# Kernel tuning notes

Hardware: AMD Instinct MI355X
Metric: run time of the kernel (lower is better)

## Reference

```python
import jax, jax.numpy as jnp
import numpy as np

N_NODES = 50000
N_EDGES = 1600000
NEG_SLOPE = 0.2


def setup_inputs() -> dict:
    key = jax.random.key(0)
    ks = jax.random.split(key, 11)
    s = 0.1  # small init scale
    return {
        "x": jax.random.normal(ks[0], (N_NODES, 128), dtype=jnp.float32),
        "edge_index": jax.random.randint(ks[1], (2, N_EDGES), 0, N_NODES, dtype=jnp.int64),
        "W1": jax.random.normal(ks[2], (128, 128), dtype=jnp.float32) * s,
        "att_src1": jax.random.normal(ks[3], (2, 64), dtype=jnp.float32) * s,
        "att_dst1": jax.random.normal(ks[4], (2, 64), dtype=jnp.float32) * s,
        "b1": jax.random.normal(ks[5], (128,), dtype=jnp.float32) * s,
        "W2": jax.random.normal(ks[6], (128, 64), dtype=jnp.float32) * s,
        "att_src2": jax.random.normal(ks[7], (1, 64), dtype=jnp.float32) * s,
        "att_dst2": jax.random.normal(ks[8], (1, 64), dtype=jnp.float32) * s,
        "b2": jax.random.normal(ks[9], (64,), dtype=jnp.float32) * s,
    }


def gat_conv(x, W, a_src, a_dst, bias, src, dst, n_nodes):
    # x: [N, F_in]; W: [F_in, H*C]; a_src/a_dst: [H, C]; bias: [H*C]
    H, C = a_src.shape
    xl = (x @ W).reshape(n_nodes, H, C)                 # [N,H,C]
    alpha_s = jnp.einsum('nhc,hc->nh', xl, a_src)       # [N,H]
    alpha_d = jnp.einsum('nhc,hc->nh', xl, a_dst)       # [N,H]
    e = jax.nn.leaky_relu(alpha_s[src] + alpha_d[dst], NEG_SLOPE)  # [E,H]
    # segment softmax over edges sharing the same destination node
    m = jax.ops.segment_max(e, dst, num_segments=n_nodes)          # [N,H]
    m = jnp.where(jnp.isfinite(m), m, 0.0)
    e = jnp.exp(e - m[dst])
    denom = jax.ops.segment_sum(e, dst, num_segments=n_nodes)      # [N,H]
    alpha = e / denom[dst]                               # self-loops guarantee denom > 0
    msg = xl[src] * alpha[:, :, None]                    # [E,H,C]
    out = jax.ops.segment_sum(msg, dst, num_segments=n_nodes)      # [N,H,C]
    return out.reshape(n_nodes, H * C) + bias


def reference(x, edge_index, W1, att_src1, att_dst1, b1, W2, att_src2, att_dst2, b2):
    n = x.shape[0]
    # PyG GATConv default add_self_loops=True
    loops = jnp.arange(n, dtype=edge_index.dtype)
    src = jnp.concatenate([edge_index[0], loops])
    dst = jnp.concatenate([edge_index[1], loops])

    h = gat_conv(x, W1, att_src1, att_dst1, b1, src, dst, n)   # [N, 128]
    h = jax.nn.relu(h)                                          # dropout p=0 (eval)
    h = gat_conv(h, W2, att_src2, att_dst2, b2, src, dst, n)   # [N, 64]
    h = jax.nn.relu(h)
    return h
```

## Files before the change

kernel.cpp:

```cpp
#include <hip/hip_runtime.h>
#include <cstdint>
#include <cstddef>

#define NEG_SLOPE 0.2f

#define NB 512
#define LOG_NB 9
#define MAXK 512

__device__ inline unsigned short f2bf(float f) {
    unsigned int u = __float_as_uint(f);
    u += 0x7FFFu + ((u >> 16) & 1u);
    return (unsigned short)(u >> 16);
}
__device__ inline float bf_lo(unsigned int u) { return __uint_as_float(u << 16); }
__device__ inline float bf_hi(unsigned int u) { return __uint_as_float(u & 0xFFFF0000u); }

__global__ __launch_bounds__(256) void sort_count_kernel(const int* __restrict__ ei, int E,
                                                         int K, int CH, int* __restrict__ bcnt) {
    __shared__ int hist[4 * MAXK];
    int tid = threadIdx.x;
    int wiw = tid >> 6;
    for (int i = tid; i < K; i += 256) {
        hist[i] = 0; hist[MAXK + i] = 0; hist[2 * MAXK + i] = 0; hist[3 * MAXK + i] = 0;
    }
    __syncthreads();
    int lo = blockIdx.x * CH;
    int hi = lo + CH; if (hi > E) hi = E;
    for (int e = lo + tid; e < hi; e += 256)
        atomicAdd(&hist[wiw * MAXK + (ei[(size_t)E + e] >> LOG_NB)], 1);
    __syncthreads();
    for (int i = tid; i < K; i += 256) {
        int c = hist[i] + hist[MAXK + i] + hist[2 * MAXK + i] + hist[3 * MAXK + i];
        if (c) atomicAdd(&bcnt[i], c);
    }
}

__global__ void sort_scan_kernel(const int* __restrict__ bcnt, int* __restrict__ boff,
                                 int* __restrict__ bcur, int K, int E) {
    __shared__ int buf[MAXK];
    int tid = threadIdx.x;
    int v = (tid < K) ? bcnt[tid] : 0;
    buf[tid] = v;
    __syncthreads();
    for (int o = 1; o < MAXK; o <<= 1) {
        int t = (tid >= o) ? buf[tid - o] : 0;
        __syncthreads();
        buf[tid] += t;
        __syncthreads();
    }
    if (tid < K) {
        int ex = buf[tid] - v;
        boff[tid] = ex;
        bcur[tid] = ex;
    }
    if (tid == K) boff[K] = E;
}


template <int FOUT, int H, int ROWS>
__device__ __forceinline__ void gemm_att_body(const float* __restrict__ X,
                                              const float* __restrict__ W,
                                              const float* __restrict__ attS,
                                              const float* __restrict__ attD,
                                              unsigned short* __restrict__ Ybf,
                                              float* __restrict__ as_,
                                              float* __restrict__ ad_, int N, int bid,
                                              float* sX, float* sW) {
    constexpr int CG  = FOUT / 4;
    constexpr int RR  = (ROWS * FOUT) / 1024;
    constexpr int LDX = 36;
    int tid = threadIdx.x;
    int rowbase = bid * ROWS;
    int cg = tid % CG;
    int rg = tid / CG;
    int r0 = rg * RR;

    float acc[RR][4];
#pragma unroll
    for (int i = 0; i < RR; i++)
#pragma unroll
        for (int c = 0; c < 4; c++) acc[i][c] = 0.f;

    for (int k0 = 0; k0 < 128; k0 += 32) {
        __syncthreads();
        for (int idx = tid; idx < ROWS * 8; idx += 256) {
            int r = idx >> 3, q = idx & 7;
            int row = rowbase + r;
            float4 val = (row < N) ? *(const float4*)&X[(size_t)row * 128 + k0 + q * 4]
                                   : make_float4(0.f, 0.f, 0.f, 0.f);
            *(float4*)&sX[r * LDX + q * 4] = val;
        }
        for (int idx = tid; idx < 8 * FOUT; idx += 256)
            *(float4*)&sW[idx * 4] = *(const float4*)&W[(size_t)k0 * FOUT + idx * 4];
        __syncthreads();
        for (int k = 0; k < 32; k += 4) {
            float4 xr[RR];
#pragma unroll
            for (int i = 0; i < RR; i++)
                xr[i] = *(const float4*)&sX[(r0 + i) * LDX + k];
#pragma unroll
            for (int kk = 0; kk < 4; kk++) {
                float4 wv = ((const float4*)(sW + (size_t)(k + kk) * FOUT))[cg];
#pragma unroll
                for (int i = 0; i < RR; i++) {
                    float xv = (&xr[i].x)[kk];
                    acc[i][0] = fmaf(xv, wv.x, acc[i][0]);
                    acc[i][1] = fmaf(xv, wv.y, acc[i][1]);
                    acc[i][2] = fmaf(xv, wv.z, acc[i][2]);
                    acc[i][3] = fmaf(xv, wv.w, acc[i][3]);
                }
            }
        }
    }

#pragma unroll
    for (int i = 0; i < RR; i++) {
        int row = rowbase + r0 + i;
        if (row < N) {
            ushort4 v;
            v.x = f2bf(acc[i][0]); v.y = f2bf(acc[i][1]);
            v.z = f2bf(acc[i][2]); v.w = f2bf(acc[i][3]);
            *(ushort4*)(Ybf + (size_t)row * FOUT + cg * 4) = v;
        }
    }

    float4 asv = ((const float4*)attS)[cg];
    float4 adv = ((const float4*)attD)[cg];
    int head = (H == 2) ? (cg >> 4) : 0;
#pragma unroll
    for (int i = 0; i < RR; i++) {
        float ps = acc[i][0] * asv.x + acc[i][1] * asv.y + acc[i][2] * asv.z + acc[i][3] * asv.w;
        float pd = acc[i][0] * adv.x + acc[i][1] * adv.y + acc[i][2] * adv.z + acc[i][3] * adv.w;
#pragma unroll
        for (int o = 1; o <= 8; o <<= 1) { ps += __shfl_xor(ps, o); pd += __shfl_xor(pd, o); }
        int row = rowbase + r0 + i;
        if ((tid & 15) == 0 && row < N) {
            as_[(size_t)row * H + head] = ps;
            ad_[(size_t)row * H + head] = pd;
        }
    }
}

__global__ __launch_bounds__(256) void scatter_gemm1_kernel(const int* __restrict__ ei, int E,
                                                            int K, int CH, int* __restrict__ bcur,
                                                            unsigned int* __restrict__ bkt,
                                                            const float* __restrict__ X,
                                                            const float* __restrict__ W1,
                                                            const float* __restrict__ attS,
                                                            const float* __restrict__ attD,
                                                            unsigned short* __restrict__ Ybf,
                                                            float* __restrict__ as_,
                                                            float* __restrict__ ad_, int N, int G) {
    __shared__ float sX[64 * 36];
    __shared__ float sW[32 * 128];
    if (blockIdx.x < G) {
        int* hist = (int*)sX;
        int* base = (int*)sW;
        int* cur2 = (int*)sW + MAXK;
        int tid = threadIdx.x;
        int wiw = tid >> 6;
        for (int i = tid; i < K; i += 256) {
            hist[i] = 0; hist[MAXK + i] = 0; hist[2 * MAXK + i] = 0; hist[3 * MAXK + i] = 0;
        }
        __syncthreads();
        int lo = blockIdx.x * CH;
        int hi = lo + CH; if (hi > E) hi = E;
        for (int e = lo + tid; e < hi; e += 256)
            atomicAdd(&hist[wiw * MAXK + (ei[(size_t)E + e] >> LOG_NB)], 1);
        __syncthreads();
        for (int i = tid; i < K; i += 256) {
            int c = hist[i] + hist[MAXK + i] + hist[2 * MAXK + i] + hist[3 * MAXK + i];
            base[i] = c ? atomicAdd(&bcur[i], c) : 0;
            cur2[i] = 0;
        }
        __syncthreads();
        for (int e = lo + tid; e < hi; e += 256) {
            int s = ei[e];
            int d = ei[(size_t)E + e];
            int k = d >> LOG_NB;
            int r = atomicAdd(&cur2[k], 1);
            bkt[(size_t)base[k] + r] = (unsigned int)s | ((unsigned int)d << 16);
        }
    } else {
        gemm_att_body<128, 2, 64>(X, W1, attS, attD, Ybf, as_, ad_, N, blockIdx.x - G, sX, sW);
    }
}

__global__ __launch_bounds__(256) void gemm2_kernel(const float* __restrict__ X,
                                                    const float* __restrict__ W,
                                                    const float* __restrict__ attS,
                                                    const float* __restrict__ attD,
                                                    unsigned short* __restrict__ Ybf,
                                                    float* __restrict__ as_,
                                                    float* __restrict__ ad_, int N) {
    __shared__ float sX[64 * 36];
    __shared__ float sW[32 * 64];
    gemm_att_body<64, 1, 64>(X, W, attS, attD, Ybf, as_, ad_, N, blockIdx.x, sX, sW);
}

__global__ __launch_bounds__(256) void sort_finalize_kernel(const unsigned int* __restrict__ bkt,
                                                            const int* __restrict__ boff,
                                                            int* __restrict__ off,
                                                            unsigned int* __restrict__ csrc, int N) {
    __shared__ int nhist[4 * NB];
    __shared__ int part[256];
    __shared__ int loff[NB];
    int k = blockIdx.x;
    int tid = threadIdx.x;
    int wiw = tid >> 6;
    int node0 = k << LOG_NB;
    int nh = N - node0; if (nh > NB) nh = NB;
    int beg = boff[k], end = boff[k + 1];
    for (int i = tid; i < NB; i += 256) {
        nhist[i] = 0; nhist[NB + i] = 0; nhist[2 * NB + i] = 0; nhist[3 * NB + i] = 0;
    }
    __syncthreads();
    for (int e = beg + tid; e < end; e += 256)
        atomicAdd(&nhist[wiw * NB + ((bkt[e] >> 16) - node0)], 1);
    __syncthreads();
    int i0 = 2 * tid, i1 = 2 * tid + 1;
    int v0 = (i0 < nh) ? nhist[i0] + nhist[NB + i0] + nhist[2 * NB + i0] + nhist[3 * NB + i0] + 1 : 0;
    int v1 = (i1 < nh) ? nhist[i1] + nhist[NB + i1] + nhist[2 * NB + i1] + nhist[3 * NB + i1] + 1 : 0;
    part[tid] = v0 + v1;
    __syncthreads();
    for (int o = 1; o < 256; o <<= 1) {
        int t = (tid >= o) ? part[tid - o] : 0;
        __syncthreads();
        part[tid] += t;
        __syncthreads();
    }
    int gbase = beg + node0;
    int base = gbase + ((tid > 0) ? part[tid - 1] : 0);
    if (i0 < nh) loff[i0] = base;
    if (i1 < nh) loff[i1] = base + v0;
    __syncthreads();
    for (int i = tid; i < nh; i += 256) {
        int node = node0 + i;
        off[node] = loff[i];
        csrc[loff[i]] = (unsigned int)node | ((unsigned int)node << 16);
        nhist[i] = loff[i] + 1;
    }
    if (node0 + nh == N && tid == 0) off[N] = gbase + part[255];
    __syncthreads();
    for (int e = beg + tid; e < end; e += 256) {
        unsigned int p = bkt[e];
        int pos = atomicAdd(&nhist[(p >> 16) - node0], 1);
        csrc[pos] = p;
    }
}


__global__ __launch_bounds__(256) void agg1_kernel(const unsigned short* __restrict__ xl,
                                                   const float* __restrict__ as_,
                                                   const float* __restrict__ ad_,
                                                   const float* __restrict__ bias,
                                                   const int* __restrict__ off,
                                                   const unsigned int* __restrict__ csrc,
                                                   float* __restrict__ out, int N) {
    __shared__ float4 sps[4][64];
    int wiw  = threadIdx.x >> 6;
    int lane = threadIdx.x & 63;
    int node = blockIdx.x * 4 + wiw;
    if (node >= N) return;
    int beg = off[node], end = off[node + 1];
    int deg = end - beg;
    float2 adn = ((const float2*)ad_)[node];

    int cl  = lane & 15;
    int sub = lane >> 4;
    int hd1 = (cl >> 3) & 1;
    float acc[8];
#pragma unroll
    for (int i = 0; i < 8; i++) acc[i] = 0.f;
    const char* xbase = (const char*)xl + cl * 16;

    if (deg <= 64) {
        int so = 0;
        float t0 = -1e30f, t1 = -1e30f;
        if (lane < deg) {
            int s = (int)(csrc[beg + lane] & 0xFFFFu);
            so = s << 8;
            float2 asv = ((const float2*)as_)[s];
            t0 = asv.x + adn.x; t0 = t0 > 0.f ? t0 : NEG_SLOPE * t0;
            t1 = asv.y + adn.y; t1 = t1 > 0.f ? t1 : NEG_SLOPE * t1;
        }
        float m0 = t0, m1 = t1;
#pragma unroll
        for (int o = 32; o; o >>= 1) {
            m0 = fmaxf(m0, __shfl_xor(m0, o));
            m1 = fmaxf(m1, __shfl_xor(m1, o));
        }
        float e0 = (lane < deg) ? __expf(t0 - m0) : 0.f;
        float e1 = (lane < deg) ? __expf(t1 - m1) : 0.f;
        float s0 = e0, s1 = e1;
#pragma unroll
        for (int o = 32; o; o >>= 1) { s0 += __shfl_xor(s0, o); s1 += __shfl_xor(s1, o); }
        sps[wiw][lane] = make_float4(e0 / s0, e1 / s1, __int_as_float(so), 0.f);
        int iters = (deg + 3) >> 2;
#pragma unroll 8
        for (int j = 0; j < iters; j++) {
            float4 q = sps[wiw][j * 4 + sub];
            float a  = hd1 ? q.y : q.x;
            uint4 v  = *(const uint4*)(xbase + __float_as_int(q.z));
            acc[0] = fmaf(a, bf_lo(v.x), acc[0]); acc[1] = fmaf(a, bf_hi(v.x), acc[1]);
            acc[2] = fmaf(a, bf_lo(v.y), acc[2]); acc[3] = fmaf(a, bf_hi(v.y), acc[3]);
            acc[4] = fmaf(a, bf_lo(v.z), acc[4]); acc[5] = fmaf(a, bf_hi(v.z), acc[5]);
            acc[6] = fmaf(a, bf_lo(v.w), acc[6]); acc[7] = fmaf(a, bf_hi(v.w), acc[7]);
        }
    } else {
        float m0 = -1e30f, m1 = -1e30f;
        for (int b = beg; b < end; b += 64) {
            int e = b + lane;
            if (e < end) {
                int s = (int)(csrc[e] & 0xFFFFu);
                float2 asv = ((const float2*)as_)[s];
                float t0 = asv.x + adn.x; t0 = t0 > 0.f ? t0 : NEG_SLOPE * t0;
                float t1 = asv.y + adn.y; t1 = t1 > 0.f ? t1 : NEG_SLOPE * t1;
                m0 = fmaxf(m0, t0); m1 = fmaxf(m1, t1);
            }
        }
#pragma unroll
        for (int o = 32; o; o >>= 1) {
            m0 = fmaxf(m0, __shfl_xor(m0, o));
            m1 = fmaxf(m1, __shfl_xor(m1, o));
        }
        float s0 = 0.f, s1 = 0.f;
        for (int b = beg; b < end; b += 64) {
            int e = b + lane;
            if (e < end) {
                int s = (int)(csrc[e] & 0xFFFFu);
                float2 asv = ((const float2*)as_)[s];
                float t0 = asv.x + adn.x; t0 = t0 > 0.f ? t0 : NEG_SLOPE * t0;
                float t1 = asv.y + adn.y; t1 = t1 > 0.f ? t1 : NEG_SLOPE * t1;
                s0 += __expf(t0 - m0); s1 += __expf(t1 - m1);
            }
        }
#pragma unroll
        for (int o = 32; o; o >>= 1) { s0 += __shfl_xor(s0, o); s1 += __shfl_xor(s1, o); }
        float i0 = 1.f / s0, i1 = 1.f / s1;
        for (int b = beg; b < end; b += 64) {
            int cnt = end - b; if (cnt > 64) cnt = 64;
            float p0 = 0.f, p1 = 0.f; int so = 0;
            if (lane < cnt) {
                int s = (int)(csrc[b + lane] & 0xFFFFu);
                so = s << 8;
                float2 asv = ((const float2*)as_)[s];
                float t0 = asv.x + adn.x; t0 = t0 > 0.f ? t0 : NEG_SLOPE * t0;
                float t1 = asv.y + adn.y; t1 = t1 > 0.f ? t1 : NEG_SLOPE * t1;
                p0 = __expf(t0 - m0) * i0; p1 = __expf(t1 - m1) * i1;
            }
            sps[wiw][lane] = make_float4(p0, p1, __int_as_float(so), 0.f);
            int iters = (cnt + 3) >> 2;
#pragma unroll 8
            for (int j = 0; j < iters; j++) {
                float4 q = sps[wiw][j * 4 + sub];
                float a  = hd1 ? q.y : q.x;
                uint4 v  = *(const uint4*)(xbase + __float_as_int(q.z));
                acc[0] = fmaf(a, bf_lo(v.x), acc[0]); acc[1] = fmaf(a, bf_hi(v.x), acc[1]);
                acc[2] = fmaf(a, bf_lo(v.y), acc[2]); acc[3] = fmaf(a, bf_hi(v.y), acc[3]);
                acc[4] = fmaf(a, bf_lo(v.z), acc[4]); acc[5] = fmaf(a, bf_hi(v.z), acc[5]);
                acc[6] = fmaf(a, bf_lo(v.w), acc[6]); acc[7] = fmaf(a, bf_hi(v.w), acc[7]);
            }
        }
    }
#pragma unroll
    for (int o = 16; o <= 32; o <<= 1)
#pragma unroll
        for (int i = 0; i < 8; i++) acc[i] += __shfl_xor(acc[i], o);
    if (sub == 0) {
        float* op = out + (size_t)node * 128 + cl * 8;
        const float* bp = bias + cl * 8;
#pragma unroll
        for (int i = 0; i < 8; i++) op[i] = fmaxf(acc[i] + bp[i], 0.f);
    }
}


__global__ __launch_bounds__(256) void agg2_kernel(const unsigned short* __restrict__ xl,
                                                   const float* __restrict__ as_,
                                                   const float* __restrict__ ad_,
                                                   const float* __restrict__ bias,
                                                   const int* __restrict__ off,
                                                   const unsigned int* __restrict__ csrc,
                                                   float* __restrict__ out, int N) {
    __shared__ float2 sps[4][64];
    int wiw  = threadIdx.x >> 6;
    int lane = threadIdx.x & 63;
    int node = blockIdx.x * 4 + wiw;
    if (node >= N) return;
    int beg = off[node], end = off[node + 1];
    int deg = end - beg;
    float adn = ad_[node];

    int cl  = lane & 7;
    int sub = lane >> 3;
    float acc[8];
#pragma unroll
    for (int i = 0; i < 8; i++) acc[i] = 0.f;
    const char* xbase = (const char*)xl + cl * 16;

    if (deg <= 64) {
        int so = 0;
        float t = -1e30f;
        if (lane < deg) {
            int s = (int)(csrc[beg + lane] & 0xFFFFu);
            so = s << 7;
            t = as_[s] + adn;
            t = t > 0.f ? t : NEG_SLOPE * t;
        }
        float m = t;
#pragma unroll
        for (int o = 32; o; o >>= 1) m = fmaxf(m, __shfl_xor(m, o));
        float evv = (lane < deg) ? __expf(t - m) : 0.f;
        float sum = evv;
#pragma unroll
        for (int o = 32; o; o >>= 1) sum += __shfl_xor(sum, o);
        sps[wiw][lane] = make_float2(evv / sum, __int_as_float(so));
        int iters = (deg + 7) >> 3;
#pragma unroll 8
        for (int j = 0; j < iters; j++) {
            float2 q = sps[wiw][j * 8 + sub];
            float a  = q.x;
            uint4 v  = *(const uint4*)(xbase + __float_as_int(q.y));
            acc[0] = fmaf(a, bf_lo(v.x), acc[0]); acc[1] = fmaf(a, bf_hi(v.x), acc[1]);
            acc[2] = fmaf(a, bf_lo(v.y), acc[2]); acc[3] = fmaf(a, bf_hi(v.y), acc[3]);
            acc[4] = fmaf(a, bf_lo(v.z), acc[4]); acc[5] = fmaf(a, bf_hi(v.z), acc[5]);
            acc[6] = fmaf(a, bf_lo(v.w), acc[6]); acc[7] = fmaf(a, bf_hi(v.w), acc[7]);
        }
    } else {
        float m = -1e30f;
        for (int b = beg; b < end; b += 64) {
            int e = b + lane;
            if (e < end) {
                float t = as_[csrc[e] & 0xFFFFu] + adn;
                t = t > 0.f ? t : NEG_SLOPE * t;
                m = fmaxf(m, t);
            }
        }
#pragma unroll
        for (int o = 32; o; o >>= 1) m = fmaxf(m, __shfl_xor(m, o));
        float sum = 0.f;
        for (int b = beg; b < end; b += 64) {
            int e = b + lane;
            if (e < end) {
                float t = as_[csrc[e] & 0xFFFFu] + adn;
                t = t > 0.f ? t : NEG_SLOPE * t;
                sum += __expf(t - m);
            }
        }
#pragma unroll
        for (int o = 32; o; o >>= 1) sum += __shfl_xor(sum, o);
        float inv = 1.f / sum;
        for (int b = beg; b < end; b += 64) {
            int cnt = end - b; if (cnt > 64) cnt = 64;
            float p = 0.f; int so = 0;
            if (lane < cnt) {
                int s = (int)(csrc[b + lane] & 0xFFFFu);
                so = s << 7;
                float t = as_[s] + adn;
                t = t > 0.f ? t : NEG_SLOPE * t;
                p = __expf(t - m) * inv;
            }
            sps[wiw][lane] = make_float2(p, __int_as_float(so));
            int iters = (cnt + 7) >> 3;
#pragma unroll 8
            for (int j = 0; j < iters; j++) {
                float2 q = sps[wiw][j * 8 + sub];
                float a  = q.x;
                uint4 v  = *(const uint4*)(xbase + __float_as_int(q.y));
                acc[0] = fmaf(a, bf_lo(v.x), acc[0]); acc[1] = fmaf(a, bf_hi(v.x), acc[1]);
                acc[2] = fmaf(a, bf_lo(v.y), acc[2]); acc[3] = fmaf(a, bf_hi(v.y), acc[3]);
                acc[4] = fmaf(a, bf_lo(v.z), acc[4]); acc[5] = fmaf(a, bf_hi(v.z), acc[5]);
                acc[6] = fmaf(a, bf_lo(v.w), acc[6]); acc[7] = fmaf(a, bf_hi(v.w), acc[7]);
            }
        }
    }
#pragma unroll
    for (int o = 8; o <= 32; o <<= 1)
#pragma unroll
        for (int i = 0; i < 8; i++) acc[i] += __shfl_xor(acc[i], o);
    if (sub == 0) {
        float* op = out + (size_t)node * 64 + cl * 8;
        const float* bp = bias + cl * 8;
#pragma unroll
        for (int i = 0; i < 8; i++) op[i] = fmaxf(acc[i] + bp[i], 0.f);
    }
}


extern "C" void kernel_launch(void* const* d_in, const int* in_sizes, int n_in,
                              void* d_out, int out_size, void* d_ws, size_t ws_size,
                              hipStream_t stream) {
    const float* x        = (const float*)d_in[0];
    const int*   ei       = (const int*)d_in[1];
    const float* W1       = (const float*)d_in[2];
    const float* attS1    = (const float*)d_in[3];
    const float* attD1    = (const float*)d_in[4];
    const float* b1       = (const float*)d_in[5];
    const float* W2       = (const float*)d_in[6];
    const float* attS2    = (const float*)d_in[7];
    const float* attD2    = (const float*)d_in[8];
    const float* b2       = (const float*)d_in[9];
    float* out            = (float*)d_out;

    int N  = in_sizes[0] / 128;
    int E  = in_sizes[1] / 2;
    int EE = E + N;
    int K  = (N + NB - 1) >> LOG_NB;

    char* w = (char*)d_ws;
    auto alloc = [&](size_t bytes) -> void* {
        void* p = (void*)w;
        w += (bytes + 255) & ~(size_t)255;
        return p;
    };
    int*   bcnt = (int*)alloc((size_t)(K + 1) * 4);
    int*   boff = (int*)alloc((size_t)(K + 1) * 4);
    int*   bcur = (int*)alloc((size_t)(K + 1) * 4);
    int*   off  = (int*)alloc((size_t)(N + 1) * 4);
    unsigned int* csrc = (unsigned int*)alloc((size_t)EE * 4);
    unsigned int* bkt  = (unsigned int*)alloc((size_t)E * 4);
    unsigned short* xl1 = (unsigned short*)alloc((size_t)N * 128 * 2);
    float* sd1  = (float*)alloc((size_t)N * 2 * 4);
    float* dd1  = (float*)alloc((size_t)N * 2 * 4);
    float* h1   = (float*)alloc((size_t)N * 128 * 4);

    unsigned short* xl2 = xl1;
    float* sd2 = sd1;
    float* dd2 = dd1;

    hipMemsetAsync(bcnt, 0, (size_t)(K + 1) * 4, stream);

    int G   = 256;
    int CH  = (E + G - 1) / G;
    int GB1 = (N + 63) / 64;
    sort_count_kernel<<<G, 256, 0, stream>>>(ei, E, K, CH, bcnt);
    sort_scan_kernel<<<1, MAXK, 0, stream>>>(bcnt, boff, bcur, K, E);
    scatter_gemm1_kernel<<<G + GB1, 256, 0, stream>>>(ei, E, K, CH, bcur, bkt,
                                                      x, W1, attS1, attD1, xl1, sd1, dd1, N, G);
    sort_finalize_kernel<<<K, 256, 0, stream>>>(bkt, boff, off, csrc, N);

    agg1_kernel<<<(N + 3) / 4, 256, 0, stream>>>(xl1, sd1, dd1, b1, off, csrc, h1, N);

    gemm2_kernel<<<(N + 63) / 64, 256, 0, stream>>>(h1, W2, attS2, attD2, xl2, sd2, dd2, N);
    agg2_kernel<<<(N + 3) / 4, 256, 0, stream>>>(xl2, sd2, dd2, b2, off, csrc, out, N);
}
```

Before: 319.1 us.

## Process two destination nodes per wavefront in both aggregation kernels

Each wavefront in agg1 and agg2 now handles two adjacent destination nodes, interleaving their softmax reductions and their gather-accumulate loops. This gives each lane two independent gather streams, raising memory-level parallelism and amortising per-node setup, and it halves the grid size. It also changes the sort bucket width (NB) from 512 to 128 nodes. The risks are higher register pressure from the doubled accumulators and divergence when the two nodes' degrees differ.

```diff
diff --git a/kernel.cpp b/kernel.cpp
--- a/kernel.cpp
+++ b/kernel.cpp
@@ -4,8 +4,8 @@
 
 #define NEG_SLOPE 0.2f
 
-#define NB 512
-#define LOG_NB 9
+#define NB 128
+#define LOG_NB 7
 #define MAXK 512
 
 __device__ inline unsigned short f2bf(float f) {
@@ -250,6 +250,64 @@
     }
 }
 
+__device__ void agg1_node_slow(const char* xbase, const float* as_, float2 adn,
+                               const unsigned int* csrc, int beg, int end,
+                               int lane, int sub, int hd1, float4* scratch, float* acc) {
+    float m0 = -1e30f, m1 = -1e30f;
+    for (int b = beg; b < end; b += 64) {
+        int e = b + lane;
+        if (e < end) {
+            int s = (int)(csrc[e] & 0xFFFFu);
+            float2 asv = ((const float2*)as_)[s];
+            float t0 = asv.x + adn.x; t0 = t0 > 0.f ? t0 : NEG_SLOPE * t0;
+            float t1 = asv.y + adn.y; t1 = t1 > 0.f ? t1 : NEG_SLOPE * t1;
+            m0 = fmaxf(m0, t0); m1 = fmaxf(m1, t1);
+        }
+    }
+#pragma unroll
+    for (int o = 32; o; o >>= 1) {
+        m0 = fmaxf(m0, __shfl_xor(m0, o));
+        m1 = fmaxf(m1, __shfl_xor(m1, o));
+    }
+    float s0 = 0.f, s1 = 0.f;
+    for (int b = beg; b < end; b += 64) {
+        int e = b + lane;
+        if (e < end) {
+            int s = (int)(csrc[e] & 0xFFFFu);
+            float2 asv = ((const float2*)as_)[s];
+            float t0 = asv.x + adn.x; t0 = t0 > 0.f ? t0 : NEG_SLOPE * t0;
+            float t1 = asv.y + adn.y; t1 = t1 > 0.f ? t1 : NEG_SLOPE * t1;
+            s0 += __expf(t0 - m0); s1 += __expf(t1 - m1);
+        }
+    }
+#pragma unroll
+    for (int o = 32; o; o >>= 1) { s0 += __shfl_xor(s0, o); s1 += __shfl_xor(s1, o); }
+    float i0 = 1.f / s0, i1 = 1.f / s1;
+    for (int b = beg; b < end; b += 64) {
+        int cnt = end - b; if (cnt > 64) cnt = 64;
+        float p0 = 0.f, p1 = 0.f; int so = 0;
+        if (lane < cnt) {
+            int s = (int)(csrc[b + lane] & 0xFFFFu);
+            so = s << 8;
+            float2 asv = ((const float2*)as_)[s];
+            float t0 = asv.x + adn.x; t0 = t0 > 0.f ? t0 : NEG_SLOPE * t0;
+            float t1 = asv.y + adn.y; t1 = t1 > 0.f ? t1 : NEG_SLOPE * t1;
+            p0 = __expf(t0 - m0) * i0; p1 = __expf(t1 - m1) * i1;
+        }
+        scratch[lane] = make_float4(p0, p1, __int_as_float(so), 0.f);
+        int iters = (cnt + 3) >> 2;
+#pragma unroll 8
+        for (int j = 0; j < iters; j++) {
+            float4 q = scratch[j * 4 + sub];
+            float a  = hd1 ? q.y : q.x;
+            uint4 v  = *(const uint4*)(xbase + __float_as_int(q.z));
+            acc[0] = fmaf(a, bf_lo(v.x), acc[0]); acc[1] = fmaf(a, bf_hi(v.x), acc[1]);
+            acc[2] = fmaf(a, bf_lo(v.y), acc[2]); acc[3] = fmaf(a, bf_hi(v.y), acc[3]);
+            acc[4] = fmaf(a, bf_lo(v.z), acc[4]); acc[5] = fmaf(a, bf_hi(v.z), acc[5]);
+            acc[6] = fmaf(a, bf_lo(v.w), acc[6]); acc[7] = fmaf(a, bf_hi(v.w), acc[7]);
+        }
+    }
+}
 
 __global__ __launch_bounds__(256) void agg1_kernel(const unsigned short* __restrict__ xl,
                                                    const float* __restrict__ as_,
@@ -258,124 +316,164 @@
                                                    const int* __restrict__ off,
                                                    const unsigned int* __restrict__ csrc,
                                                    float* __restrict__ out, int N) {
-    __shared__ float4 sps[4][64];
+    __shared__ float4 sps[4][2][64];
     int wiw  = threadIdx.x >> 6;
     int lane = threadIdx.x & 63;
-    int node = blockIdx.x * 4 + wiw;
-    if (node >= N) return;
-    int beg = off[node], end = off[node + 1];
-    int deg = end - beg;
-    float2 adn = ((const float2*)ad_)[node];
+    int wv   = blockIdx.x * 4 + wiw;
+    int nodeA = wv * 2;
+    if (nodeA >= N) return;
+    int nodeB = nodeA + 1;
+    bool hasB = nodeB < N;
+    int begA = off[nodeA], endA = off[nodeA + 1];
+    int degA = endA - begA;
+    int begB = endA, degB = 0;
+    if (hasB) degB = off[nodeB + 1] - endA;
+    float2 adnA = ((const float2*)ad_)[nodeA];
+    float2 adnB = hasB ? ((const float2*)ad_)[nodeB] : make_float2(0.f, 0.f);
 
     int cl  = lane & 15;
     int sub = lane >> 4;
     int hd1 = (cl >> 3) & 1;
-    float acc[8];
-#pragma unroll
-    for (int i = 0; i < 8; i++) acc[i] = 0.f;
     const char* xbase = (const char*)xl + cl * 16;
-
-    if (deg <= 64) {
-        int so = 0;
-        float t0 = -1e30f, t1 = -1e30f;
-        if (lane < deg) {
-            int s = (int)(csrc[beg + lane] & 0xFFFFu);
-            so = s << 8;
-            float2 asv = ((const float2*)as_)[s];
-            t0 = asv.x + adn.x; t0 = t0 > 0.f ? t0 : NEG_SLOPE * t0;
-            t1 = asv.y + adn.y; t1 = t1 > 0.f ? t1 : NEG_SLOPE * t1;
-        }
-        float m0 = t0, m1 = t1;
+    float accA[8], accB[8];
+#pragma unroll
+    for (int i = 0; i < 8; i++) { accA[i] = 0.f; accB[i] = 0.f; }
+
+    if (degA <= 64 && degB <= 64) {
+        int soA = 0, soB = 0;
+        float tA0 = -1e30f, tA1 = -1e30f, tB0 = -1e30f, tB1 = -1e30f;
+        if (lane < degA) {
+            int s = (int)(csrc[begA + lane] & 0xFFFFu);
+            soA = s << 8;
+            float2 a = ((const float2*)as_)[s];
+            tA0 = a.x + adnA.x; tA0 = tA0 > 0.f ? tA0 : NEG_SLOPE * tA0;
+            tA1 = a.y + adnA.y; tA1 = tA1 > 0.f ? tA1 : NEG_SLOPE * tA1;
+        }
+        if (lane < degB) {
+            int s = (int)(csrc[begB + lane] & 0xFFFFu);
+            soB = s << 8;
+            float2 a = ((const float2*)as_)[s];
+            tB0 = a.x + adnB.x; tB0 = tB0 > 0.f ? tB0 : NEG_SLOPE * tB0;
+            tB1 = a.y + adnB.y; tB1 = tB1 > 0.f ? tB1 : NEG_SLOPE * tB1;
+        }
+        float mA0 = tA0, mA1 = tA1, mB0 = tB0, mB1 = tB1;
 #pragma unroll
         for (int o = 32; o; o >>= 1) {
-            m0 = fmaxf(m0, __shfl_xor(m0, o));
-            m1 = fmaxf(m1, __shfl_xor(m1, o));
-        }
-        float e0 = (lane < deg) ? __expf(t0 - m0) : 0.f;
-        float e1 = (lane < deg) ? __expf(t1 - m1) : 0.f;
-        float s0 = e0, s1 = e1;
-#pragma unroll
-        for (int o = 32; o; o >>= 1) { s0 += __shfl_xor(s0, o); s1 += __shfl_xor(s1, o); }
-        sps[wiw][lane] = make_float4(e0 / s0, e1 / s1, __int_as_float(so), 0.f);
-        int iters = (deg + 3) >> 2;
+            mA0 = fmaxf(mA0, __shfl_xor(mA0, o)); mA1 = fmaxf(mA1, __shfl_xor(mA1, o));
+            mB0 = fmaxf(mB0, __shfl_xor(mB0, o)); mB1 = fmaxf(mB1, __shfl_xor(mB1, o));
+        }
+        float eA0 = (lane < degA) ? __expf(tA0 - mA0) : 0.f;
+        float eA1 = (lane < degA) ? __expf(tA1 - mA1) : 0.f;
+        float eB0 = (lane < degB) ? __expf(tB0 - mB0) : 0.f;
+        float eB1 = (lane < degB) ? __expf(tB1 - mB1) : 0.f;
+        float sA0 = eA0, sA1 = eA1, sB0 = eB0, sB1 = eB1;
+#pragma unroll
+        for (int o = 32; o; o >>= 1) {
+            sA0 += __shfl_xor(sA0, o); sA1 += __shfl_xor(sA1, o);
+            sB0 += __shfl_xor(sB0, o); sB1 += __shfl_xor(sB1, o);
+        }
+        sps[wiw][0][lane] = make_float4(eA0 / sA0, eA1 / sA1, __int_as_float(soA), 0.f);
+        sps[wiw][1][lane] = make_float4(hasB ? eB0 / sB0 : 0.f, hasB ? eB1 / sB1 : 0.f,
+                                        __int_as_float(soB), 0.f);
+        int itersA = (degA + 3) >> 2;
+        int itersB = (degB + 3) >> 2;
+        int iters = itersA > itersB ? itersA : itersB;
+#pragma unroll 4
+        for (int j = 0; j < iters; j++) {
+            if (j < itersA) {
+                float4 q = sps[wiw][0][j * 4 + sub];
+                float a  = hd1 ? q.y : q.x;
+                uint4 v  = *(const uint4*)(xbase + __float_as_int(q.z));
+                accA[0] = fmaf(a, bf_lo(v.x), accA[0]); accA[1] = fmaf(a, bf_hi(v.x), accA[1]);
+                accA[2] = fmaf(a, bf_lo(v.y), accA[2]); accA[3] = fmaf(a, bf_hi(v.y), accA[3]);
+                accA[4] = fmaf(a, bf_lo(v.z), accA[4]); accA[5] = fmaf(a, bf_hi(v.z), accA[5]);
+                accA[6] = fmaf(a, bf_lo(v.w), accA[6]); accA[7] = fmaf(a, bf_hi(v.w), accA[7]);
+            }
+            if (j < itersB) {
+                float4 q = sps[wiw][1][j * 4 + sub];
+                float a  = hd1 ? q.y : q.x;
+                uint4 v  = *(const uint4*)(xbase + __float_as_int(q.z));
+                accB[0] = fmaf(a, bf_lo(v.x), accB[0]); accB[1] = fmaf(a, bf_hi(v.x), accB[1]);
+                accB[2] = fmaf(a, bf_lo(v.y), accB[2]); accB[3] = fmaf(a, bf_hi(v.y), accB[3]);
+                accB[4] = fmaf(a, bf_lo(v.z), accB[4]); accB[5] = fmaf(a, bf_hi(v.z), accB[5]);
+                accB[6] = fmaf(a, bf_lo(v.w), accB[6]); accB[7] = fmaf(a, bf_hi(v.w), accB[7]);
+            }
+        }
+    } else {
+        agg1_node_slow(xbase, as_, adnA, csrc, begA, endA, lane, sub, hd1, sps[wiw][0], accA);
+        if (hasB)
+            agg1_node_slow(xbase, as_, adnB, csrc, begB, begB + degB, lane, sub, hd1, sps[wiw][1], accB);
+    }
+#pragma unroll
+    for (int o = 16; o <= 32; o <<= 1)
+#pragma unroll
+        for (int i = 0; i < 8; i++) {
+            accA[i] += __shfl_xor(accA[i], o);
+            accB[i] += __shfl_xor(accB[i], o);
+        }
+    if (sub == 0) {
+        const float* bp = bias + cl * 8;
+        float* opA = out + (size_t)nodeA * 128 + cl * 8;
+#pragma unroll
+        for (int i = 0; i < 8; i++) opA[i] = fmaxf(accA[i] + bp[i], 0.f);
+        if (hasB) {
+            float* opB = out + (size_t)nodeB * 128 + cl * 8;
+#pragma unroll
+            for (int i = 0; i < 8; i++) opB[i] = fmaxf(accB[i] + bp[i], 0.f);
+        }
+    }
+}
+
+__device__ void agg2_node_slow(const char* xbase, const float* as_, float adn,
+                               const unsigned int* csrc, int beg, int end,
+                               int lane, int sub, float2* scratch, float* acc) {
+    float m = -1e30f;
+    for (int b = beg; b < end; b += 64) {
+        int e = b + lane;
+        if (e < end) {
+            float t = as_[csrc[e] & 0xFFFFu] + adn;
+            t = t > 0.f ? t : NEG_SLOPE * t;
+            m = fmaxf(m, t);
+        }
+    }
+#pragma unroll
+    for (int o = 32; o; o >>= 1) m = fmaxf(m, __shfl_xor(m, o));
+    float sum = 0.f;
+    for (int b = beg; b < end; b += 64) {
+        int e = b + lane;
+        if (e < end) {
+            float t = as_[csrc[e] & 0xFFFFu] + adn;
+            t = t > 0.f ? t : NEG_SLOPE * t;
+            sum += __expf(t - m);
+        }
+    }
+#pragma unroll
+    for (int o = 32; o; o >>= 1) sum += __shfl_xor(sum, o);
+    float inv = 1.f / sum;
+    for (int b = beg; b < end; b += 64) {
+        int cnt = end - b; if (cnt > 64) cnt = 64;
+        float p = 0.f; int so = 0;
+        if (lane < cnt) {
+            int s = (int)(csrc[b + lane] & 0xFFFFu);
+            so = s << 7;
+            float t = as_[s] + adn;
+            t = t > 0.f ? t : NEG_SLOPE * t;
+            p = __expf(t - m) * inv;
+        }
+        scratch[lane] = make_float2(p, __int_as_float(so));
+        int iters = (cnt + 7) >> 3;
 #pragma unroll 8
         for (int j = 0; j < iters; j++) {
-            float4 q = sps[wiw][j * 4 + sub];
-            float a  = hd1 ? q.y : q.x;
-            uint4 v  = *(const uint4*)(xbase + __float_as_int(q.z));
+            float2 q = scratch[j * 8 + sub];
+            float a  = q.x;
+            uint4 v  = *(const uint4*)(xbase + __float_as_int(q.y));
             acc[0] = fmaf(a, bf_lo(v.x), acc[0]); acc[1] = fmaf(a, bf_hi(v.x), acc[1]);
             acc[2] = fmaf(a, bf_lo(v.y), acc[2]); acc[3] = fmaf(a, bf_hi(v.y), acc[3]);
             acc[4] = fmaf(a, bf_lo(v.z), acc[4]); acc[5] = fmaf(a, bf_hi(v.z), acc[5]);
             acc[6] = fmaf(a, bf_lo(v.w), acc[6]); acc[7] = fmaf(a, bf_hi(v.w), acc[7]);
         }
-    } else {
-        float m0 = -1e30f, m1 = -1e30f;
-        for (int b = beg; b < end; b += 64) {
-            int e = b + lane;
-            if (e < end) {
-                int s = (int)(csrc[e] & 0xFFFFu);
-                float2 asv = ((const float2*)as_)[s];
-                float t0 = asv.x + adn.x; t0 = t0 > 0.f ? t0 : NEG_SLOPE * t0;
-                float t1 = asv.y + adn.y; t1 = t1 > 0.f ? t1 : NEG_SLOPE * t1;
-                m0 = fmaxf(m0, t0); m1 = fmaxf(m1, t1);
-            }
-        }
-#pragma unroll
-        for (int o = 32; o; o >>= 1) {
-            m0 = fmaxf(m0, __shfl_xor(m0, o));
-            m1 = fmaxf(m1, __shfl_xor(m1, o));
-        }
-        float s0 = 0.f, s1 = 0.f;
-        for (int b = beg; b < end; b += 64) {
-            int e = b + lane;
-            if (e < end) {
-                int s = (int)(csrc[e] & 0xFFFFu);
-                float2 asv = ((const float2*)as_)[s];
-                float t0 = asv.x + adn.x; t0 = t0 > 0.f ? t0 : NEG_SLOPE * t0;
-                float t1 = asv.y + adn.y; t1 = t1 > 0.f ? t1 : NEG_SLOPE * t1;
-                s0 += __expf(t0 - m0); s1 += __expf(t1 - m1);
-            }
-        }
-#pragma unroll
-        for (int o = 32; o; o >>= 1) { s0 += __shfl_xor(s0, o); s1 += __shfl_xor(s1, o); }
-        float i0 = 1.f / s0, i1 = 1.f / s1;
-        for (int b = beg; b < end; b += 64) {
-            int cnt = end - b; if (cnt > 64) cnt = 64;
-            float p0 = 0.f, p1 = 0.f; int so = 0;
-            if (lane < cnt) {
-                int s = (int)(csrc[b + lane] & 0xFFFFu);
-                so = s << 8;
-                float2 asv = ((const float2*)as_)[s];
-                float t0 = asv.x + adn.x; t0 = t0 > 0.f ? t0 : NEG_SLOPE * t0;
-                float t1 = asv.y + adn.y; t1 = t1 > 0.f ? t1 : NEG_SLOPE * t1;
-                p0 = __expf(t0 - m0) * i0; p1 = __expf(t1 - m1) * i1;
-            }
-            sps[wiw][lane] = make_float4(p0, p1, __int_as_float(so), 0.f);
-            int iters = (cnt + 3) >> 2;
-#pragma unroll 8
-            for (int j = 0; j < iters; j++) {
-                float4 q = sps[wiw][j * 4 + sub];
-                float a  = hd1 ? q.y : q.x;
-                uint4 v  = *(const uint4*)(xbase + __float_as_int(q.z));
-                acc[0] = fmaf(a, bf_lo(v.x), acc[0]); acc[1] = fmaf(a, bf_hi(v.x), acc[1]);
-                acc[2] = fmaf(a, bf_lo(v.y), acc[2]); acc[3] = fmaf(a, bf_hi(v.y), acc[3]);
-                acc[4] = fmaf(a, bf_lo(v.z), acc[4]); acc[5] = fmaf(a, bf_hi(v.z), acc[5]);
-                acc[6] = fmaf(a, bf_lo(v.w), acc[6]); acc[7] = fmaf(a, bf_hi(v.w), acc[7]);
-            }
-        }
-    }
-#pragma unroll
-    for (int o = 16; o <= 32; o <<= 1)
-#pragma unroll
-        for (int i = 0; i < 8; i++) acc[i] += __shfl_xor(acc[i], o);
-    if (sub == 0) {
-        float* op = out + (size_t)node * 128 + cl * 8;
-        const float* bp = bias + cl * 8;
-#pragma unroll
-        for (int i = 0; i < 8; i++) op[i] = fmaxf(acc[i] + bp[i], 0.f);
-    }
-}
-
+    }
+}
 
 __global__ __launch_bounds__(256) void agg2_kernel(const unsigned short* __restrict__ xl,
                                                    const float* __restrict__ as_,
@@ -384,107 +482,102 @@
                                                    const int* __restrict__ off,
                                                    const unsigned int* __restrict__ csrc,
                                                    float* __restrict__ out, int N) {
-    __shared__ float2 sps[4][64];
+    __shared__ float2 sps[4][2][64];
     int wiw  = threadIdx.x >> 6;
     int lane = threadIdx.x & 63;
-    int node = blockIdx.x * 4 + wiw;
-    if (node >= N) return;
-    int beg = off[node], end = off[node + 1];
-    int deg = end - beg;
-    float adn = ad_[node];
+    int wv   = blockIdx.x * 4 + wiw;
+    int nodeA = wv * 2;
+    if (nodeA >= N) return;
+    int nodeB = nodeA + 1;
+    bool hasB = nodeB < N;
+    int begA = off[nodeA], endA = off[nodeA + 1];
+    int degA = endA - begA;
+    int begB = endA, degB = 0;
+    if (hasB) degB = off[nodeB + 1] - endA;
+    float adnA = ad_[nodeA];
+    float adnB = hasB ? ad_[nodeB] : 0.f;
 
     int cl  = lane & 7;
     int sub = lane >> 3;
-    float acc[8];
-#pragma unroll
-    for (int i = 0; i < 8; i++) acc[i] = 0.f;
     const char* xbase = (const char*)xl + cl * 16;
-
-    if (deg <= 64) {
-        int so = 0;
-        float t = -1e30f;
-        if (lane < deg) {
-            int s = (int)(csrc[beg + lane] & 0xFFFFu);
-            so = s << 7;
-            t = as_[s] + adn;
-            t = t > 0.f ? t : NEG_SLOPE * t;
-        }
-        float m = t;
-#pragma unroll
-        for (int o = 32; o; o >>= 1) m = fmaxf(m, __shfl_xor(m, o));
-        float evv = (lane < deg) ? __expf(t - m) : 0.f;
-        float sum = evv;
-#pragma unroll
-        for (int o = 32; o; o >>= 1) sum += __shfl_xor(sum, o);
-        sps[wiw][lane] = make_float2(evv / sum, __int_as_float(so));
-        int iters = (deg + 7) >> 3;
-#pragma unroll 8
+    float accA[8], accB[8];
+#pragma unroll
+    for (int i = 0; i < 8; i++) { accA[i] = 0.f; accB[i] = 0.f; }
+
+    if (degA <= 64 && degB <= 64) {
+        int soA = 0, soB = 0;
+        float tA = -1e30f, tB = -1e30f;
+        if (lane < degA) {
+            int s = (int)(csrc[begA + lane] & 0xFFFFu);
+            soA = s << 7;
+            tA = as_[s] + adnA;
+            tA = tA > 0.f ? tA : NEG_SLOPE * tA;
+        }
+        if (lane < degB) {
+            int s = (int)(csrc[begB + lane] & 0xFFFFu);
+            soB = s << 7;
+            tB = as_[s] + adnB;
+            tB = tB > 0.f ? tB : NEG_SLOPE * tB;
+        }
+        float mA = tA, mB = tB;
+#pragma unroll
+        for (int o = 32; o; o >>= 1) {
+            mA = fmaxf(mA, __shfl_xor(mA, o));
+            mB = fmaxf(mB, __shfl_xor(mB, o));
+        }
+        float eA = (lane < degA) ? __expf(tA - mA) : 0.f;
+        float eB = (lane < degB) ? __expf(tB - mB) : 0.f;
+        float sA = eA, sB = eB;
+#pragma unroll
+        for (int o = 32; o; o >>= 1) { sA += __shfl_xor(sA, o); sB += __shfl_xor(sB, o); }
+        sps[wiw][0][lane] = make_float2(eA / sA, __int_as_float(soA));
+        sps[wiw][1][lane] = make_float2(hasB ? eB / sB : 0.f, __int_as_float(soB));
+        int itersA = (degA + 7) >> 3;
+        int itersB = (degB + 7) >> 3;
+        int iters = itersA > itersB ? itersA : itersB;
+#pragma unroll 4
         for (int j = 0; j < iters; j++) {
-            float2 q = sps[wiw][j * 8 + sub];
-            float a  = q.x;
-            uint4 v  = *(const uint4*)(xbase + __float_as_int(q.y));
-            acc[0] = fmaf(a, bf_lo(v.x), acc[0]); acc[1] = fmaf(a, bf_hi(v.x), acc[1]);
-            acc[2] = fmaf(a, bf_lo(v.y), acc[2]); acc[3] = fmaf(a, bf_hi(v.y), acc[3]);
-            acc[4] = fmaf(a, bf_lo(v.z), acc[4]); acc[5] = fmaf(a, bf_hi(v.z), acc[5]);
-            acc[6] = fmaf(a, bf_lo(v.w), acc[6]); acc[7] = fmaf(a, bf_hi(v.w), acc[7]);
-        }
-    } else {
-        float m = -1e30f;
-        for (int b = beg; b < end; b += 64) {
-            int e = b + lane;
-            if (e < end) {
-                float t = as_[csrc[e] & 0xFFFFu] + adn;
-                t = t > 0.f ? t : NEG_SLOPE * t;
-                m = fmaxf(m, t);
-            }
-        }
-#pragma unroll
-        for (int o = 32; o; o >>= 1) m = fmaxf(m, __shfl_xor(m, o));
-        float sum = 0.f;
-        for (int b = beg; b < end; b += 64) {
-            int e = b + lane;
-            if (e < end) {
-                float t = as_[csrc[e] & 0xFFFFu] + adn;
-                t = t > 0.f ? t : NEG_SLOPE * t;
-                sum += __expf(t - m);
-            }
-        }
-#pragma unroll
-        for (int o = 32; o; o >>= 1) sum += __shfl_xor(sum, o);
-        float inv = 1.f / sum;
-        for (int b = beg; b < end; b += 64) {
-            int cnt = end - b; if (cnt > 64) cnt = 64;
-            float p = 0.f; int so = 0;
-            if (lane < cnt) {
-                int s = (int)(csrc[b + lane] & 0xFFFFu);
-                so = s << 7;
-                float t = as_[s] + adn;
-                t = t > 0.f ? t : NEG_SLOPE * t;
-                p = __expf(t - m) * inv;
-            }
-            sps[wiw][lane] = make_float2(p, __int_as_float(so));
-            int iters = (cnt + 7) >> 3;
-#pragma unroll 8
-            for (int j = 0; j < iters; j++) {
-                float2 q = sps[wiw][j * 8 + sub];
+            if (j < itersA) {
+                float2 q = sps[wiw][0][j * 8 + sub];
                 float a  = q.x;
                 uint4 v  = *(const uint4*)(xbase + __float_as_int(q.y));
-                acc[0] = fmaf(a, bf_lo(v.x), acc[0]); acc[1] = fmaf(a, bf_hi(v.x), acc[1]);
-                acc[2] = fmaf(a, bf_lo(v.y), acc[2]); acc[3] = fmaf(a, bf_hi(v.y), acc[3]);
-                acc[4] = fmaf(a, bf_lo(v.z), acc[4]); acc[5] = fmaf(a, bf_hi(v.z), acc[5]);
-                acc[6] = fmaf(a, bf_lo(v.w), acc[6]); acc[7] = fmaf(a, bf_hi(v.w), acc[7]);
+                accA[0] = fmaf(a, bf_lo(v.x), accA[0]); accA[1] = fmaf(a, bf_hi(v.x), accA[1]);
+                accA[2] = fmaf(a, bf_lo(v.y), accA[2]); accA[3] = fmaf(a, bf_hi(v.y), accA[3]);
+                accA[4] = fmaf(a, bf_lo(v.z), accA[4]); accA[5] = fmaf(a, bf_hi(v.z), accA[5]);
+                accA[6] = fmaf(a, bf_lo(v.w), accA[6]); accA[7] = fmaf(a, bf_hi(v.w), accA[7]);
             }
-        }
+            if (j < itersB) {
+                float2 q = sps[wiw][1][j * 8 + sub];
+                float a  = q.x;
+                uint4 v  = *(const uint4*)(xbase + __float_as_int(q.y));
+                accB[0] = fmaf(a, bf_lo(v.x), accB[0]); accB[1] = fmaf(a, bf_hi(v.x), accB[1]);
+                accB[2] = fmaf(a, bf_lo(v.y), accB[2]); accB[3] = fmaf(a, bf_hi(v.y), accB[3]);
+                accB[4] = fmaf(a, bf_lo(v.z), accB[4]); accB[5] = fmaf(a, bf_hi(v.z), accB[5]);
+                accB[6] = fmaf(a, bf_lo(v.w), accB[6]); accB[7] = fmaf(a, bf_hi(v.w), accB[7]);
+            }
+        }
+    } else {
+        agg2_node_slow(xbase, as_, adnA, csrc, begA, endA, lane, sub, sps[wiw][0], accA);
+        if (hasB)
+            agg2_node_slow(xbase, as_, adnB, csrc, begB, begB + degB, lane, sub, sps[wiw][1], accB);
     }
 #pragma unroll
     for (int o = 8; o <= 32; o <<= 1)
 #pragma unroll
-        for (int i = 0; i < 8; i++) acc[i] += __shfl_xor(acc[i], o);
+        for (int i = 0; i < 8; i++) {
+            accA[i] += __shfl_xor(accA[i], o);
+            accB[i] += __shfl_xor(accB[i], o);
+        }
     if (sub == 0) {
-        float* op = out + (size_t)node * 64 + cl * 8;
         const float* bp = bias + cl * 8;
-#pragma unroll
-        for (int i = 0; i < 8; i++) op[i] = fmaxf(acc[i] + bp[i], 0.f);
+        float* opA = out + (size_t)nodeA * 64 + cl * 8;
+#pragma unroll
+        for (int i = 0; i < 8; i++) opA[i] = fmaxf(accA[i] + bp[i], 0.f);
+        if (hasB) {
+            float* opB = out + (size_t)nodeB * 64 + cl * 8;
+#pragma unroll
+            for (int i = 0; i < 8; i++) opB[i] = fmaxf(accB[i] + bp[i], 0.f);
+        }
     }
 }
 
@@ -541,8 +634,8 @@
                                                       x, W1, attS1, attD1, xl1, sd1, dd1, N, G);
     sort_finalize_kernel<<<K, 256, 0, stream>>>(bkt, boff, off, csrc, N);
 
-    agg1_kernel<<<(N + 3) / 4, 256, 0, stream>>>(xl1, sd1, dd1, b1, off, csrc, h1, N);
+    agg1_kernel<<<(N + 7) / 8, 256, 0, stream>>>(xl1, sd1, dd1, b1, off, csrc, h1, N);
 
     gemm2_kernel<<<(N + 63) / 64, 256, 0, stream>>>(h1, W2, attS2, attD2, xl2, sd2, dd2, N);
-    agg2_kernel<<<(N + 3) / 4, 256, 0, stream>>>(xl2, sd2, dd2, b2, off, csrc, out, N);
-}
+    agg2_kernel<<<(N + 7) / 8, 256, 0, stream>>>(xl2, sd2, dd2, b2, off, csrc, out, N);
+}
```

Measured after the change: 310.0 us. 1.03x faster.
